# Kernel optimization log

Measured on AMD Instinct MI355X. Metric: run time of the kernel, lower is better.

Reference implementation:

```python
import jax, jax.numpy as jnp
import numpy as np

D_MODEL = 1024
NUM_HEADS = 16
HEAD_DIM = D_MODEL // NUM_HEADS  # 64
SEQ = 2048
BATCH = 4
LN_EPS = 1e-5


def setup_inputs() -> dict:
    key = jax.random.key(0)
    k_in, k_qkv, k_o, k_g = jax.random.split(key, 4)
    inputs = jax.random.normal(k_in, (BATCH, SEQ, D_MODEL), dtype=jnp.float32)
    mask = jnp.zeros((BATCH, 1, SEQ, SEQ), dtype=jnp.float32)  # additive mask
    # Realistic rotary embeddings (RoPE), duplicated-halves layout
    inv_freq = 1.0 / (10000.0 ** (jnp.arange(0, HEAD_DIM, 2, dtype=jnp.float32) / HEAD_DIM))
    pos = jnp.arange(SEQ, dtype=jnp.float32)
    freqs = pos[:, None] * inv_freq[None, :]            # [S, Dh/2]
    emb = jnp.concatenate([freqs, freqs], axis=-1)       # [S, Dh]
    cos = jnp.cos(emb)
    sin = jnp.sin(emb)
    # Parameters
    sd = 1.0 / np.sqrt(D_MODEL)
    w_qkv = jax.random.normal(k_qkv, (D_MODEL, 3 * D_MODEL), dtype=jnp.float32) * sd
    w_o = jax.random.normal(k_o, (D_MODEL, D_MODEL), dtype=jnp.float32) * sd
    ln_gamma = jnp.ones((D_MODEL,), dtype=jnp.float32)
    return {"inputs": inputs, "mask": mask, "cos": cos, "sin": sin,
            "ln_gamma": ln_gamma, "w_qkv": w_qkv, "w_o": w_o}


def _rotate_half(x):
    x1, x2 = jnp.split(x, 2, axis=-1)
    return jnp.concatenate([-x2, x1], axis=-1)


def reference(inputs, mask, cos, sin, ln_gamma, w_qkv, w_o):
    B, S, D = inputs.shape
    # Pre-attention LayerNorm (layer_id != 0), center=False -> no beta
    mu = jnp.mean(inputs, axis=-1, keepdims=True)
    var = jnp.mean(jnp.square(inputs - mu), axis=-1, keepdims=True)
    x = (inputs - mu) / jnp.sqrt(var + LN_EPS) * ln_gamma
    # Fused QKV projection, split into heads: [B, H, S, Dh]
    qkv = (x @ w_qkv).reshape(B, S, 3, NUM_HEADS, HEAD_DIM)
    qkv = jnp.transpose(qkv, (2, 0, 3, 1, 4))
    q, k, v = qkv[0], qkv[1], qkv[2]
    # RoPE
    c = cos.reshape(1, 1, S, HEAD_DIM)
    s = sin.reshape(1, 1, S, HEAD_DIM)
    q = q * c + _rotate_half(q) * s
    k = k * c + _rotate_half(k) * s
    # Scaled dot-product attention with additive mask
    scale = 1.0 / jnp.sqrt(jnp.asarray(HEAD_DIM, dtype=q.dtype))
    logits = jnp.einsum("bhqd,bhkd->bhqk", q, k) * scale + mask
    attn = jax.nn.softmax(logits, axis=-1)
    out = jnp.einsum("bhqk,bhkd->bhqd", attn, v)
    out = jnp.transpose(out, (0, 2, 1, 3)).reshape(B, S, D)
    return out @ w_o
```

## Files before the change

### kernel.cpp

```cpp
#include <hip/hip_runtime.h>
#include <stdint.h>

#define DEV __device__ __forceinline__

typedef __bf16 bf16x8 __attribute__((ext_vector_type(8)));
typedef float f32x4 __attribute__((ext_vector_type(4)));
typedef float f32x16 __attribute__((ext_vector_type(16)));

DEV unsigned short f2bf(float f) {
  union { float f; uint32_t u; } c; c.f = f;
  uint32_t u = c.u;
  u += 0x7FFFu + ((u >> 16) & 1u);
  return (unsigned short)(u >> 16);
}
DEV float bf2f(unsigned short h) {
  union { uint32_t u; float f; } c; c.u = ((uint32_t)h) << 16;
  return c.f;
}
DEV float u2f(uint32_t u) {
  union { uint32_t u; float f; } c; c.u = u;
  return c.f;
}
DEV bf16x8 ld8(const unsigned short* p) {
  uint4 u = *reinterpret_cast<const uint4*>(p);
  return __builtin_bit_cast(bf16x8, u);
}
DEV uint32_t cvtpk(float lo, float hi) {
  uint32_t r;
  asm("v_cvt_pk_bf16_f32 %0, %1, %2" : "=v"(r) : "v"(lo), "v"(hi));
  return r;
}
DEV void permswap(uint32_t& a, uint32_t& b) {
  asm("v_permlane32_swap_b32 %0, %1" : "+v"(a), "+v"(b));
}
DEV float exp2b(float x) { return __builtin_amdgcn_exp2f(x); }
DEV void gload16(const void* g, void* l) {
  __builtin_amdgcn_global_load_lds((const __attribute__((address_space(1))) void*)g,
                                   (__attribute__((address_space(3))) void*)l, 16, 0, 0);
}

template<int K, int N>
__global__ __launch_bounds__(256)
void transpose_cast_kernel(const float* __restrict__ in, unsigned short* __restrict__ out) {
  __shared__ float tile[64][65];
  const int bk = blockIdx.x % (K / 64);
  const int bn = blockIdx.x / (K / 64);
  const int k0 = bk * 64, n0 = bn * 64;
  const int t = threadIdx.x;
#pragma unroll
  for (int i = 0; i < 16; ++i) {
    int idx = t + i * 256;
    int kl = idx >> 6, nl = idx & 63;
    tile[kl][nl] = in[(size_t)(k0 + kl) * N + n0 + nl];
  }
  __syncthreads();
#pragma unroll
  for (int i = 0; i < 16; ++i) {
    int idx = t + i * 256;
    int nl = idx >> 6, kl = idx & 63;
    out[(size_t)(n0 + nl) * K + k0 + kl] = f2bf(tile[kl][nl]);
  }
}

__global__ __launch_bounds__(256)
void ln_kernel(const float* __restrict__ x, const float* __restrict__ gamma,
               unsigned short* __restrict__ y) {
  const int row = blockIdx.x;
  const int t = threadIdx.x;
  const float4 v = reinterpret_cast<const float4*>(x + (size_t)row * 1024)[t];
  float s  = v.x + v.y + v.z + v.w;
  float s2 = v.x * v.x + v.y * v.y + v.z * v.z + v.w * v.w;
#pragma unroll
  for (int off = 1; off < 64; off <<= 1) {
    s  += __shfl_xor(s, off);
    s2 += __shfl_xor(s2, off);
  }
  __shared__ float red[8];
  const int w = t >> 6, lane = t & 63;
  if (lane == 0) { red[w] = s; red[4 + w] = s2; }
  __syncthreads();
  s  = red[0] + red[1] + red[2] + red[3];
  s2 = red[4] + red[5] + red[6] + red[7];
  const float mu = s * (1.0f / 1024.0f);
  const float var = s2 * (1.0f / 1024.0f) - mu * mu;
  const float rstd = rsqrtf(var + 1e-5f);
  const float4 g = reinterpret_cast<const float4*>(gamma)[t];
  ushort4 o;
  o.x = f2bf((v.x - mu) * rstd * g.x);
  o.y = f2bf((v.y - mu) * rstd * g.y);
  o.z = f2bf((v.z - mu) * rstd * g.z);
  o.w = f2bf((v.w - mu) * rstd * g.w);
  reinterpret_cast<ushort4*>(y + (size_t)row * 1024)[t] = o;
}

template<int N_DIM, bool OUT_F32>
__global__ __launch_bounds__(256)
void gemm_bt_kernel(const unsigned short* __restrict__ A,
                    const unsigned short* __restrict__ Bt,
                    void* __restrict__ Cout) {
  constexpr int K = 1024;
  __shared__ unsigned short a_lds[128 * 32];
  __shared__ unsigned short b_lds[128 * 32];
  const int t = threadIdx.x;
  const int w = t >> 6, l = t & 63;
  const int lrow = l & 15, lch = l >> 4;
  const int nbn = N_DIM / 128;
  const int m0 = (blockIdx.x / nbn) * 128;
  const int n0 = (blockIdx.x % nbn) * 128;
  const int wm = (w >> 1) * 64, wn = (w & 1) * 64;

  const int srow = t >> 2;
  const int schk = t & 3;
  const int scol = ((schk ^ (srow & 3)) << 3);
  const unsigned short* aS0 = A  + (size_t)(m0 + srow) * K + scol;
  const unsigned short* aS1 = A  + (size_t)(m0 + 64 + srow) * K + scol;
  const unsigned short* bS0 = Bt + (size_t)(n0 + srow) * K + scol;
  const unsigned short* bS1 = Bt + (size_t)(n0 + 64 + srow) * K + scol;
  unsigned short* aD0 = a_lds + (w * 16) * 32;
  unsigned short* aD1 = a_lds + (64 + w * 16) * 32;
  unsigned short* bD0 = b_lds + (w * 16) * 32;
  unsigned short* bD1 = b_lds + (64 + w * 16) * 32;

  f32x4 acc[4][4] = {};

  for (int k0 = 0; k0 < K; k0 += 32) {
    gload16(aS0 + k0, aD0);
    gload16(aS1 + k0, aD1);
    gload16(bS0 + k0, bD0);
    gload16(bS1 + k0, bD1);
    __syncthreads();
    bf16x8 af[4], bfr[4];
#pragma unroll
    for (int m = 0; m < 4; ++m) {
      int row = wm + m * 16 + lrow;
      af[m] = ld8(a_lds + row * 32 + ((lch ^ (lrow & 3)) << 3));
    }
#pragma unroll
    for (int n = 0; n < 4; ++n) {
      int row = wn + n * 16 + lrow;
      bfr[n] = ld8(b_lds + row * 32 + ((lch ^ (lrow & 3)) << 3));
    }
#pragma unroll
    for (int m = 0; m < 4; ++m)
#pragma unroll
      for (int n = 0; n < 4; ++n)
        acc[m][n] = __builtin_amdgcn_mfma_f32_16x16x32_bf16(af[m], bfr[n], acc[m][n], 0, 0, 0);
    __syncthreads();
  }

#pragma unroll
  for (int m = 0; m < 4; ++m) {
    const int grow0 = m0 + wm + m * 16 + lch * 4;
#pragma unroll
    for (int n = 0; n < 4; ++n) {
      const int gcol = n0 + wn + n * 16 + lrow;
#pragma unroll
      for (int r = 0; r < 4; ++r) {
        if constexpr (OUT_F32)
          ((float*)Cout)[(size_t)(grow0 + r) * N_DIM + gcol] = acc[m][n][r];
        else
          ((unsigned short*)Cout)[(size_t)(grow0 + r) * N_DIM + gcol] = f2bf(acc[m][n][r]);
      }
    }
  }
}

__global__ __launch_bounds__(256)
void rope_split_kernel(const unsigned short* __restrict__ qkv,
                       const float* __restrict__ cosb,
                       const float* __restrict__ sinb,
                       unsigned short* __restrict__ Qo,
                       unsigned short* __restrict__ Kf,
                       unsigned short* __restrict__ Vf) {
  const int bid = blockIdx.x;
  const int sb = bid & 31, h = (bid >> 5) & 15, b = bid >> 9;
  const int s0 = sb * 64;
  const int t = threadIdx.x;
  __shared__ unsigned short qt[64][72], kt[64][72], vt[64][72];

  const int sl = t >> 2, c0 = (t & 3) * 16;
  {
    const size_t base = (size_t)(b * 2048 + s0 + sl) * 3072 + h * 64 + c0;
    uint4 q1 = *(const uint4*)(qkv + base);
    uint4 q2 = *(const uint4*)(qkv + base + 8);
    uint4 k1 = *(const uint4*)(qkv + base + 1024);
    uint4 k2 = *(const uint4*)(qkv + base + 1032);
    uint4 v1 = *(const uint4*)(qkv + base + 2048);
    uint4 v2 = *(const uint4*)(qkv + base + 2056);
    *(uint4*)&qt[sl][c0] = q1; *(uint4*)&qt[sl][c0 + 8] = q2;
    *(uint4*)&kt[sl][c0] = k1; *(uint4*)&kt[sl][c0 + 8] = k2;
    *(uint4*)&vt[sl][c0] = v1; *(uint4*)&vt[sl][c0 + 8] = v2;
  }
  __syncthreads();
  const size_t fbase = (size_t)(b * 16 + h) * 131072;
  {
    const int sg = s0 + sl;
    alignas(16) unsigned short qo16[16], ko16[16];
#pragma unroll
    for (int j = 0; j < 16; ++j) {
      const int d = c0 + j;
      const float cv = cosb[sg * 64 + d], sv = sinb[sg * 64 + d];
      const float qv = bf2f(qt[sl][d]), qp = bf2f(qt[sl][d ^ 32]);
      const float kv = bf2f(kt[sl][d]), kp = bf2f(kt[sl][d ^ 32]);
      const float rq = qv * cv + ((d < 32) ? -qp : qp) * sv;
      const float rk = kv * cv + ((d < 32) ? -kp : kp) * sv;
      qo16[j] = f2bf(rq * 0.180336880f);
      ko16[j] = f2bf(rk);
    }
    const size_t ob = ((size_t)(b * 16 + h) * 2048 + sg) * 64 + c0;
    *(uint4*)(Qo + ob) = *(uint4*)qo16; *(uint4*)(Qo + ob + 8) = *(uint4*)(qo16 + 8);
    unsigned short* kd = Kf + fbase + ((size_t)((sb * 2 + (sl >> 5)) * 4 + (t & 3))) * 512;
    *(uint4*)(kd + (sl & 31) * 8)        = *(uint4*)ko16;
    *(uint4*)(kd + (32 + (sl & 31)) * 8) = *(uint4*)(ko16 + 8);
  }
  {
    const int dh = t >> 2, sc0 = (t & 3) * 16;
    alignas(16) unsigned short vo16[16];
#pragma unroll
    for (int j = 0; j < 16; ++j) vo16[j] = vt[sc0 + j][dh];
    unsigned short* vd = Vf + fbase + ((size_t)((sb * 2 + (dh >> 5)) * 4 + (t & 3))) * 512;
    *(uint4*)(vd + (dh & 31) * 8)        = *(uint4*)vo16;
    *(uint4*)(vd + (32 + (dh & 31)) * 8) = *(uint4*)(vo16 + 8);
  }
}

__global__ __launch_bounds__(256)
void mask_prep_kernel(const float* __restrict__ mask, unsigned short* __restrict__ mrs,
                      unsigned char* __restrict__ flg) {
  const int bid = blockIdx.x;
  const int kvt = bid & 31, qc = (bid >> 5) & 31, b = bid >> 10;
  const int t = threadIdx.x;
  __shared__ float tile[64][72];
  __shared__ int nzf;
  if (t == 0) nzf = 0;
  uint32_t orbits = 0;
  {
    const int r = t >> 2, c0 = (t & 3) * 16;
    const float* src = mask + (size_t)b * (2048ull * 2048) + (size_t)(qc * 64 + r) * 2048 + kvt * 64 + c0;
#pragma unroll
    for (int i = 0; i < 4; ++i) {
      const float4 v = *(const float4*)(src + i * 4);
      *(float4*)&tile[r][c0 + i * 4] = v;
      orbits |= __float_as_uint(v.x) | __float_as_uint(v.y) |
                __float_as_uint(v.z) | __float_as_uint(v.w);
    }
  }
  __syncthreads();
  if (orbits != 0u) nzf = 1;
  __syncthreads();
  if (nzf) {
    const int cid = t >> 5;
    const int n = cid >> 2, jj = (cid >> 1) & 1, hi = cid & 1;
    const int qq0 = (t & 31) * 2;
    const int cb = n * 32 + jj * 16 + hi * 4;
    unsigned short* dst = mrs + (((size_t)(b * 32 + kvt) * 8 + cid) * 2048 + qc * 64) * 8;
#pragma unroll
    for (int qo = 0; qo < 2; ++qo) {
      const int q = qq0 + qo;
      alignas(16) unsigned short o8[8];
#pragma unroll
      for (int v = 0; v < 8; ++v) {
        const int col = cb + (v >> 2) * 8 + (v & 3);
        o8[v] = f2bf(tile[q][col] * 1.44269504f);
      }
      *(uint4*)(dst + (size_t)q * 8) = *(uint4*)o8;
    }
  }
  if (t == 0) flg[(size_t)(b * 32 + kvt) * 32 + qc] = (unsigned char)nzf;
}

__global__ __launch_bounds__(256)
void attn_kernel(const unsigned short* __restrict__ Q,
                 const unsigned short* __restrict__ Kf,
                 const unsigned short* __restrict__ Vf,
                 const unsigned short* __restrict__ mrs,
                 const unsigned char* __restrict__ flg,
                 unsigned short* __restrict__ O) {
  const int t = threadIdx.x, w = t >> 6, l = t & 63;
  const int lq = l & 31, hi = l >> 5;
  const int bid = blockIdx.x;
  const int x = bid & 7, y = bid >> 3;
  const int bh = x * 8 + (y >> 4);
  const int qb = y & 15;
  const int b = bh >> 4, h = bh & 15;
  const int q0 = qb * 128 + w * 32;

  const unsigned short* Qb  = Q  + (size_t)bh * (2048 * 64);
  const unsigned short* Kfb = Kf + (size_t)bh * 131072 + l * 8;
  const unsigned short* Vfb = Vf + (size_t)bh * 131072 + l * 8;
  const unsigned short* ml = mrs + (size_t)b * 4194304 + (size_t)hi * 16384 + (size_t)(q0 + lq) * 8;
  const unsigned char* fb = flg + (size_t)(b * 32) * 32 + qb * 2;

  bf16x8 qf[4];
  {
    const unsigned short* qp = Qb + (size_t)(q0 + lq) * 64 + hi * 8;
#pragma unroll
    for (int c = 0; c < 4; ++c) qf[c] = ld8(qp + c * 16);
  }
  bf16x8 ones;
  {
    const uint4 ou = { 0x3F803F80u, 0x3F803F80u, 0x3F803F80u, 0x3F803F80u };
    ones = __builtin_bit_cast(bf16x8, ou);
  }

  f32x16 ot0 = {}, ot1 = {};
  f32x16 st_sum = {};

  unsigned int bmap = 0;
  for (int kvt = 0; kvt < 32; ++kvt)
    if (fb[kvt * 32] | fb[kvt * 32 + 1]) bmap |= (1u << kvt);

  uint4 krA[8], krB[8];
#pragma unroll
  for (int i = 0; i < 8; ++i) krA[i] = *(const uint4*)(Kfb + i * 512);

  auto do_tile = [&](int kvt, uint4 (&ckr)[8], uint4 (&nkr)[8], bool hm) {
    if (kvt + 1 < 32) {
      const unsigned short* kp = Kfb + (size_t)(kvt + 1) * 4096;
#pragma unroll
      for (int i = 0; i < 8; ++i) nkr[i] = *(const uint4*)(kp + i * 512);
    }
    const unsigned short* vp = Vfb + (size_t)kvt * 4096;
    uint4 vr[8];
#pragma unroll
    for (int i = 0; i < 8; ++i) vr[i] = *(const uint4*)(vp + i * 512);

    f32x16 st0 = {}, st1 = {};
    if (hm) {
      const unsigned short* mp = ml + (size_t)kvt * 131072;
      uint4 mc[4];
#pragma unroll
      for (int c2 = 0; c2 < 4; ++c2) mc[c2] = *(const uint4*)(mp + c2 * 32768);
#pragma unroll
      for (int jj = 0; jj < 2; ++jj) {
        const uint4 u0 = mc[jj];
        const uint4 u1 = mc[2 + jj];
#pragma unroll
        for (int wv = 0; wv < 4; ++wv) {
          const uint32_t w0 = ((const uint32_t*)&u0)[wv];
          const uint32_t w1 = ((const uint32_t*)&u1)[wv];
          st0[jj * 8 + wv * 2]     = u2f(w0 << 16);
          st0[jj * 8 + wv * 2 + 1] = u2f(w0 & 0xffff0000u);
          st1[jj * 8 + wv * 2]     = u2f(w1 << 16);
          st1[jj * 8 + wv * 2 + 1] = u2f(w1 & 0xffff0000u);
        }
      }
    }

    __builtin_amdgcn_s_setprio(1);
#pragma unroll
    for (int c = 0; c < 4; ++c) {
      st0 = __builtin_amdgcn_mfma_f32_32x32x16_bf16(__builtin_bit_cast(bf16x8, ckr[c]),     qf[c], st0, 0, 0, 0);
      st1 = __builtin_amdgcn_mfma_f32_32x32x16_bf16(__builtin_bit_cast(bf16x8, ckr[4 + c]), qf[c], st1, 0, 0, 0);
    }
    __builtin_amdgcn_s_setprio(0);

#pragma unroll
    for (int r = 0; r < 16; ++r) {
      st0[r] = exp2b(st0[r]);
      st1[r] = exp2b(st1[r]);
    }

    bf16x8 pa[4];
#pragma unroll
    for (int c = 0; c < 4; ++c) {
      const int e8 = (c & 1) * 8;
      uint32_t A01, B01, A23, B23;
      if (c < 2) {
        A01 = cvtpk(st0[e8 + 0], st0[e8 + 1]);
        B01 = cvtpk(st0[e8 + 4], st0[e8 + 5]);
        A23 = cvtpk(st0[e8 + 2], st0[e8 + 3]);
        B23 = cvtpk(st0[e8 + 6], st0[e8 + 7]);
      } else {
        A01 = cvtpk(st1[e8 + 0], st1[e8 + 1]);
        B01 = cvtpk(st1[e8 + 4], st1[e8 + 5]);
        A23 = cvtpk(st1[e8 + 2], st1[e8 + 3]);
        B23 = cvtpk(st1[e8 + 6], st1[e8 + 7]);
      }
      permswap(A01, B01);
      permswap(A23, B23);
      const uint4 pw = { A01, A23, B01, B23 };
      pa[c] = __builtin_bit_cast(bf16x8, pw);
    }

    __builtin_amdgcn_s_setprio(1);
#pragma unroll
    for (int c = 0; c < 4; ++c) {
      ot0 = __builtin_amdgcn_mfma_f32_32x32x16_bf16(__builtin_bit_cast(bf16x8, vr[c]),     pa[c], ot0, 0, 0, 0);
      ot1 = __builtin_amdgcn_mfma_f32_32x32x16_bf16(__builtin_bit_cast(bf16x8, vr[4 + c]), pa[c], ot1, 0, 0, 0);
      st_sum = __builtin_amdgcn_mfma_f32_32x32x16_bf16(ones, pa[c], st_sum, 0, 0, 0);
    }
    __builtin_amdgcn_s_setprio(0);
  };

  for (int kvt = 0; kvt < 32; kvt += 2) {
    do_tile(kvt,     krA, krB, (bmap >> kvt) & 1u);
    do_tile(kvt + 1, krB, krA, (bmap >> (kvt + 1)) & 1u);
  }

  const float inv = 1.0f / st_sum[0];
  unsigned short* ob = O + ((size_t)(b * 2048 + q0 + lq) * 16 + h) * 64 + hi * 4;
#pragma unroll
  for (int td = 0; td < 2; ++td) {
#pragma unroll
    for (int rr = 0; rr < 4; ++rr) {
      ushort4 ov;
      if (td == 0) {
        ov.x = f2bf(ot0[rr * 4 + 0] * inv);
        ov.y = f2bf(ot0[rr * 4 + 1] * inv);
        ov.z = f2bf(ot0[rr * 4 + 2] * inv);
        ov.w = f2bf(ot0[rr * 4 + 3] * inv);
      } else {
        ov.x = f2bf(ot1[rr * 4 + 0] * inv);
        ov.y = f2bf(ot1[rr * 4 + 1] * inv);
        ov.z = f2bf(ot1[rr * 4 + 2] * inv);
        ov.w = f2bf(ot1[rr * 4 + 3] * inv);
      }
      *(ushort4*)(ob + td * 32 + rr * 8) = ov;
    }
  }
}

extern "C" void kernel_launch(void* const* d_in, const int* in_sizes, int n_in,
                              void* d_out, int out_size, void* d_ws, size_t ws_size,
                              hipStream_t stream) {
  (void)in_sizes; (void)n_in; (void)out_size; (void)ws_size;
  const float* x     = (const float*)d_in[0];
  const float* mask  = (const float*)d_in[1];
  const float* cosb  = (const float*)d_in[2];
  const float* sinb  = (const float*)d_in[3];
  const float* gamma = (const float*)d_in[4];
  const float* w_qkv = (const float*)d_in[5];
  const float* w_o   = (const float*)d_in[6];

  char* ws = (char*)d_ws;
  unsigned short* x_bf   = (unsigned short*)(ws);
  unsigned short* wqkvT  = (unsigned short*)(ws + 16777216);
  unsigned short* woT    = (unsigned short*)(ws + 23068672);
  unsigned short* qkv_bf = (unsigned short*)(ws + 25165824);
  unsigned short* q_r    = (unsigned short*)(ws + 75497472);
  unsigned short* k_f    = (unsigned short*)(ws + 92274688);
  unsigned short* v_f    = (unsigned short*)(ws + 109051904);
  unsigned short* attn   = (unsigned short*)(ws + 125829120);
  unsigned short* mask_rs = qkv_bf;
  unsigned char*  flags   = (unsigned char*)(ws + 25165824 + 33554432);

  transpose_cast_kernel<1024, 3072><<<dim3(16 * 48), dim3(256), 0, stream>>>(w_qkv, wqkvT);
  transpose_cast_kernel<1024, 1024><<<dim3(16 * 16), dim3(256), 0, stream>>>(w_o, woT);
  ln_kernel<<<dim3(8192), dim3(256), 0, stream>>>(x, gamma, x_bf);
  gemm_bt_kernel<3072, false><<<dim3(64 * 24), dim3(256), 0, stream>>>(x_bf, wqkvT, (void*)qkv_bf);
  rope_split_kernel<<<dim3(4 * 16 * 32), dim3(256), 0, stream>>>(qkv_bf, cosb, sinb, q_r, k_f, v_f);
  mask_prep_kernel<<<dim3(4096), dim3(256), 0, stream>>>(mask, mask_rs, flags);
  attn_kernel<<<dim3(1024), dim3(256), 0, stream>>>(q_r, k_f, v_f, mask_rs, flags, attn);
  gemm_bt_kernel<1024, true><<<dim3(64 * 8), dim3(256), 0, stream>>>(attn, woT, d_out);
}
```

Before: 257.6 us.

## Stage K/V tiles through double-buffered LDS shared across waves

Replaces per-wave register prefetch of K and V tiles from global memory with cooperative global-to-LDS loads, where each wave fetches two chunks into a double buffer. All four waves then read the tile from LDS. The aim is to cut redundant global/L2 traffic, since each wave previously loaded the full K and V tile itself. It adds a block-wide barrier per KV tile, 32 KB of LDS per block, and LDS read latency inside the loop.

```diff
diff --git a/kernel.cpp b/kernel.cpp
--- a/kernel.cpp
+++ b/kernel.cpp
@@ -291,6 +291,9 @@
   const unsigned short* ml = mrs + (size_t)b * 4194304 + (size_t)hi * 16384 + (size_t)(q0 + lq) * 8;
   const unsigned char* fb = flg + (size_t)(b * 32) * 32 + qb * 2;
 
+  __shared__ unsigned short k_lds[2][4096];
+  __shared__ unsigned short v_lds[2][4096];
+
   bf16x8 qf[4];
   {
     const unsigned short* qp = Qb + (size_t)(q0 + lq) * 64 + hi * 8;
@@ -305,25 +308,39 @@
 
   f32x16 ot0 = {}, ot1 = {};
   f32x16 st_sum = {};
+  int cur = 0;
 
   unsigned int bmap = 0;
   for (int kvt = 0; kvt < 32; ++kvt)
     if (fb[kvt * 32] | fb[kvt * 32 + 1]) bmap |= (1u << kvt);
 
-  uint4 krA[8], krB[8];
-#pragma unroll
-  for (int i = 0; i < 8; ++i) krA[i] = *(const uint4*)(Kfb + i * 512);
-
-  auto do_tile = [&](int kvt, uint4 (&ckr)[8], uint4 (&nkr)[8], bool hm) {
+  const int ch0 = w * 2;
+  gload16(Kfb + (size_t)(ch0)     * 512, k_lds[0] + (ch0)     * 512);
+  gload16(Kfb + (size_t)(ch0 + 1) * 512, k_lds[0] + (ch0 + 1) * 512);
+  gload16(Vfb + (size_t)(ch0)     * 512, v_lds[0] + (ch0)     * 512);
+  gload16(Vfb + (size_t)(ch0 + 1) * 512, v_lds[0] + (ch0 + 1) * 512);
+  __syncthreads();
+
+  for (int kvt = 0; kvt < 32; ++kvt) {
+    const bool hm = (bmap >> kvt) & 1u;
     if (kvt + 1 < 32) {
-      const unsigned short* kp = Kfb + (size_t)(kvt + 1) * 4096;
-#pragma unroll
-      for (int i = 0; i < 8; ++i) nkr[i] = *(const uint4*)(kp + i * 512);
-    }
-    const unsigned short* vp = Vfb + (size_t)kvt * 4096;
-    uint4 vr[8];
-#pragma unroll
-    for (int i = 0; i < 8; ++i) vr[i] = *(const uint4*)(vp + i * 512);
+      const unsigned short* kS = Kfb + (size_t)(kvt + 1) * 4096;
+      const unsigned short* vS = Vfb + (size_t)(kvt + 1) * 4096;
+      unsigned short* kD = k_lds[cur ^ 1];
+      unsigned short* vD = v_lds[cur ^ 1];
+      gload16(kS + (size_t)(ch0)     * 512, kD + (ch0)     * 512);
+      gload16(kS + (size_t)(ch0 + 1) * 512, kD + (ch0 + 1) * 512);
+      gload16(vS + (size_t)(ch0)     * 512, vD + (ch0)     * 512);
+      gload16(vS + (size_t)(ch0 + 1) * 512, vD + (ch0 + 1) * 512);
+    }
+
+    const unsigned short* kb = k_lds[cur] + l * 8;
+    const unsigned short* vb = v_lds[cur] + l * 8;
+    bf16x8 kfr[8], vfr[8];
+#pragma unroll
+    for (int i = 0; i < 8; ++i) kfr[i] = ld8(kb + i * 512);
+#pragma unroll
+    for (int i = 0; i < 8; ++i) vfr[i] = ld8(vb + i * 512);
 
     f32x16 st0 = {}, st1 = {};
     if (hm) {
@@ -350,8 +367,8 @@
     __builtin_amdgcn_s_setprio(1);
 #pragma unroll
     for (int c = 0; c < 4; ++c) {
-      st0 = __builtin_amdgcn_mfma_f32_32x32x16_bf16(__builtin_bit_cast(bf16x8, ckr[c]),     qf[c], st0, 0, 0, 0);
-      st1 = __builtin_amdgcn_mfma_f32_32x32x16_bf16(__builtin_bit_cast(bf16x8, ckr[4 + c]), qf[c], st1, 0, 0, 0);
+      st0 = __builtin_amdgcn_mfma_f32_32x32x16_bf16(kfr[c],     qf[c], st0, 0, 0, 0);
+      st1 = __builtin_amdgcn_mfma_f32_32x32x16_bf16(kfr[4 + c], qf[c], st1, 0, 0, 0);
     }
     __builtin_amdgcn_s_setprio(0);
 
@@ -386,16 +403,14 @@
     __builtin_amdgcn_s_setprio(1);
 #pragma unroll
     for (int c = 0; c < 4; ++c) {
-      ot0 = __builtin_amdgcn_mfma_f32_32x32x16_bf16(__builtin_bit_cast(bf16x8, vr[c]),     pa[c], ot0, 0, 0, 0);
-      ot1 = __builtin_amdgcn_mfma_f32_32x32x16_bf16(__builtin_bit_cast(bf16x8, vr[4 + c]), pa[c], ot1, 0, 0, 0);
+      ot0 = __builtin_amdgcn_mfma_f32_32x32x16_bf16(vfr[c],     pa[c], ot0, 0, 0, 0);
+      ot1 = __builtin_amdgcn_mfma_f32_32x32x16_bf16(vfr[4 + c], pa[c], ot1, 0, 0, 0);
       st_sum = __builtin_amdgcn_mfma_f32_32x32x16_bf16(ones, pa[c], st_sum, 0, 0, 0);
     }
     __builtin_amdgcn_s_setprio(0);
-  };
-
-  for (int kvt = 0; kvt < 32; kvt += 2) {
-    do_tile(kvt,     krA, krB, (bmap >> kvt) & 1u);
-    do_tile(kvt + 1, krB, krA, (bmap >> (kvt + 1)) & 1u);
+
+    __syncthreads();
+    cur ^= 1;
   }
 
   const float inv = 1.0f / st_sum[0];
```

Result: faster. 251.3 us (-2.4%).
